# Kernel optimization log

Measured on AMD Instinct MI355X. Metric: run time of the kernel, lower is better.

Reference implementation:

```python
import jax, jax.numpy as jnp
import numpy as np

B, NPROP, NCLS, NPTS, NBQ, NCK = 32, 256, 19, 4096, 64, 64
C, QH, VQ = 256, 768, 8


def setup_inputs() -> dict:
    key = jax.random.key(0)
    ks = jax.random.split(key, 12)
    s = 0.02
    return dict(
        sem_cls_logits=jax.random.normal(ks[0], (B, NPROP, NCLS), jnp.float32),
        prop_features=jax.random.normal(ks[1], (B, NPROP, C), jnp.float32),
        box_corners=jax.random.normal(ks[2], (B, NPROP, 8, 3), jnp.float32),
        enc_xyz=jax.random.uniform(ks[3], (B, NPTS, 3), jnp.float32),
        enc_features=jax.random.normal(ks[4], (B, NPTS, C), jnp.float32),
        pc_min=jnp.zeros((B, 3), jnp.float32),
        pc_max=jnp.ones((B, 3), jnp.float32),
        box_query=jax.random.normal(ks[5], (B, NBQ, 8, 3), jnp.float32),
        box_qmask=jnp.ones((B, NBQ), jnp.float32),
        click_query=jax.random.uniform(ks[6], (B, NCK, 3), jnp.float32),
        click_qmask=jnp.ones((B, NCK), jnp.float32),
        gauss_B=jax.random.normal(ks[7], (3, C // 2), jnp.float32),
        box_w1=jax.random.normal(ks[8], (C, QH), jnp.float32) * s,
        box_b1=jnp.zeros((QH,), jnp.float32),
        box_w2=jax.random.normal(ks[9], (QH, VQ * QH), jnp.float32) * s,
        box_b2=jnp.zeros((VQ * QH,), jnp.float32),
        click_w1=jax.random.normal(ks[10], (2 * C, QH), jnp.float32) * s,
        click_b1=jnp.zeros((QH,), jnp.float32),
        click_w2=jax.random.normal(ks[11], (QH, VQ * QH), jnp.float32) * s,
        click_b2=jnp.zeros((VQ * QH,), jnp.float32),
    )


def _mlp(x, w1, b1, w2, b2):
    h = jax.nn.relu(jnp.einsum('bqc,ch->bqh', x, w1) + b1)
    return jnp.einsum('bqh,ho->bqo', h, w2) + b2


def _forward(sem_cls_logits, prop_features, box_corners, enc_xyz, enc_features,
             pc_min, pc_max, box_query, box_qmask, click_query, click_qmask,
             gauss_B, box_w1, box_b1, box_w2, box_b2,
             click_w1, click_b1, click_w2, click_b2):
    bsz = sem_cls_logits.shape[0]
    # proposal semantic mask: 0 for background (last class)
    prop_sem_mask = (jnp.argmax(sem_cls_logits, -1) != sem_cls_logits.shape[-1] - 1)
    prop_sem_mask = prop_sem_mask.astype(prop_features.dtype)  # [B, nprop]

    # ---- box branch: axis-aligned 3D IoU from box corners, argmax match, gather ----
    mn_p = box_corners.min(-2)  # [B, nprop, 3]
    mx_p = box_corners.max(-2)
    vol_p = jnp.prod(mx_p - mn_p, -1)  # [B, nprop]
    mn_q = box_query.min(-2)   # [B, nq, 3]
    mx_q = box_query.max(-2)
    vol_q = jnp.prod(mx_q - mn_q, -1)  # [B, nq]
    inter = jnp.prod(
        jnp.clip(jnp.minimum(mx_q[:, :, None], mx_p[:, None]) -
                 jnp.maximum(mn_q[:, :, None], mn_p[:, None]), 0.0, None), -1)  # [B,nq,nprop]
    iou = inter / (vol_q[:, :, None] + vol_p[:, None] - inter + 1e-8)
    iou = iou * prop_sem_mask[:, None, :]
    match_idx = jnp.argmax(iou, -1)  # [B, nq]
    box_feat = jnp.take_along_axis(prop_features, match_idx[..., None], axis=1)  # [B,nq,C]
    box_prompt = _mlp(box_feat, box_w1, box_b1, box_w2, box_b2).reshape(bsz, -1, QH)
    box_mask = jnp.repeat(box_qmask[:, :, None], VQ, axis=2).reshape(bsz, -1)

    # ---- click branch: fourier pos emb + nearest-neighbor gather + MLP ----
    xyz01 = (click_query - pc_min[:, None]) / (pc_max - pc_min)[:, None]
    proj = (xyz01 * (2.0 * jnp.pi)) @ gauss_B  # [B, nclick, C//2]
    pos = jnp.concatenate([jnp.sin(proj), jnp.cos(proj)], -1)  # [B, nclick, C]
    # squared distances (argmin equivalent to cdist argmin)
    d2 = jnp.sum((click_query[:, :, None, :] - enc_xyz[:, None, :, :]) ** 2, -1)  # [B,nclick,npts]
    nn_ids = jnp.argmin(d2, -1)  # [B, nclick]
    k_fea = jnp.take_along_axis(enc_features, nn_ids[..., None], axis=1)  # [B,nclick,C]
    click_in = jnp.concatenate([k_fea, pos], -1)  # [B, nclick, 2C]
    click_prompt = _mlp(click_in, click_w1, click_b1, click_w2, click_b2).reshape(bsz, -1, QH)
    click_mask = jnp.repeat(click_qmask[:, :, None], VQ, axis=2).reshape(bsz, -1)

    prompt_feature = jnp.concatenate([box_prompt, click_prompt], axis=1)  # [B,(nq+nclick)*VQ,QH]
    prompt_mask = jnp.concatenate([box_mask, click_mask], axis=1)
    return prompt_feature, prompt_mask


def reference(sem_cls_logits, prop_features, box_corners, enc_xyz, enc_features,
              pc_min, pc_max, box_query, box_qmask, click_query, click_qmask,
              gauss_B, box_w1, box_b1, box_w2, box_b2,
              click_w1, click_b1, click_w2, click_b2):
    return _forward(sem_cls_logits, prop_features, box_corners, enc_xyz, enc_features,
                    pc_min, pc_max, box_query, box_qmask, click_query, click_qmask,
                    gauss_B, box_w1, box_b1, box_w2, box_b2,
                    click_w1, click_b1, click_w2, click_b2)
```

## Files before the change

### kernel.cpp

```cpp
#include <hip/hip_runtime.h>

#define TWO_PI 6.283185307179586f

typedef _Float16 half8 __attribute__((ext_vector_type(8)));
typedef _Float16 half4 __attribute__((ext_vector_type(4)));
typedef float floatx4 __attribute__((ext_vector_type(4)));

__device__ __forceinline__ void async16(const _Float16* g, _Float16* l) {
    __builtin_amdgcn_global_load_lds(
        (const __attribute__((address_space(1))) void*)g,
        (__attribute__((address_space(3))) void*)l, 16, 0, 0);
}

__device__ __forceinline__ void transpose_core(
    const float* __restrict__ src, _Float16* __restrict__ dst,
    int K, int N, _Float16* t, int bx, int by)
{
    int n0 = bx * 64, k0 = by * 64;
    int tid = threadIdx.x;
    int r = tid >> 4;
    int c4 = (tid & 15) * 4;
#pragma unroll
    for (int p = 0; p < 4; p++) {
        int k = r + p*16;
        float4 v = *(const float4*)(src + (size_t)(k0+k)*N + n0 + c4);
        t[(c4+0)*68 + k] = (_Float16)v.x;
        t[(c4+1)*68 + k] = (_Float16)v.y;
        t[(c4+2)*68 + k] = (_Float16)v.z;
        t[(c4+3)*68 + k] = (_Float16)v.w;
    }
    __syncthreads();
    int ck = (tid & 15) * 4;
#pragma unroll
    for (int p = 0; p < 4; p++) {
        int n = r + p*16;
        half4 v = *(const half4*)(t + n*68 + ck);
        *(half4*)(dst + (size_t)(n0+n)*K + k0 + ck) = v;
    }
}

__global__ void mega_prep(
    const float* __restrict__ logits, const float* __restrict__ corners,
    const float* __restrict__ box_query,
    const float* __restrict__ bw1, const float* __restrict__ cw1,
    _Float16* __restrict__ w1t_box, _Float16* __restrict__ w1t_clk,
    const float* __restrict__ bw2, const float* __restrict__ cw2,
    _Float16* __restrict__ w2t_box, _Float16* __restrict__ w2t_clk,
    const float* __restrict__ prop_features,
    const float* __restrict__ enc_features,
    const float* __restrict__ enc_xyz,
    const float* __restrict__ cq,
    const float* __restrict__ pc_min,
    const float* __restrict__ pc_max,
    const float* __restrict__ gB,
    const float* __restrict__ box_qmask,
    const float* __restrict__ click_qmask,
    _Float16* __restrict__ box_in,
    _Float16* __restrict__ click_in,
    float* __restrict__ out)
{
    __shared__ float smem[2176];
    __shared__ float nnd[4]; __shared__ int nni[4];
    __shared__ float bxd[4]; __shared__ int bxi[4];
    __shared__ int s_nn, s_match;
    int bid = blockIdx.x;
    if (bid < 2304) {
        _Float16* tb = (_Float16*)smem;
        int x = bid % 96, y = (bid / 96) % 12, z = bid / 1152;
        if (z == 0) transpose_core(bw2, w2t_box, 768, 6144, tb, x, y);
        else        transpose_core(cw2, w2t_clk, 768, 6144, tb, x, y);
        return;
    }
    if (bid < 2496) {
        _Float16* tb = (_Float16*)smem;
        int r = bid - 2304;
        int x = r % 12, y = (r / 12) % 8, z = r / 96;
        if (z == 0) {
            if (y < 4) transpose_core(bw1, w1t_box, 256, 768, tb, x, y);
        } else {
            transpose_core(cw1, w1t_clk, 512, 768, tb, x, y);
        }
        return;
    }

    int row = bid - 2496;
    int t = threadIdx.x;
    int b = row >> 6;
    int lane = t & 63, wave = t >> 6;

    float cx = cq[row*3+0];
    float cy = cq[row*3+1];
    float cz = cq[row*3+2];
    const float* ex = enc_xyz + (size_t)b * 4096 * 3;
    float nbest = 3.4e38f; int nbidx = 0;
#pragma unroll
    for (int i = 0; i < 16; i++) {
        int p = t + i*256;
        float dx = cx - ex[p*3+0];
        float dy = cy - ex[p*3+1];
        float dz = cz - ex[p*3+2];
        float d = dx*dx + dy*dy;
        d = d + dz*dz;
        if (d < nbest) { nbest = d; nbidx = p; }
    }
#pragma unroll
    for (int off = 32; off; off >>= 1) {
        float ov = __shfl_down(nbest, off);
        int   oi = __shfl_down(nbidx, off);
        if (ov < nbest || (ov == nbest && oi < nbidx)) { nbest = ov; nbidx = oi; }
    }
    if (lane == 0) { nnd[wave] = nbest; nni[wave] = nbidx; }

    float iou; int pidx = t;
    {
        const float* c = corners + ((size_t)b*256 + t) * 24;
        float mn0 = c[0], mn1 = c[1], mn2 = c[2];
        float mx0 = mn0, mx1 = mn1, mx2 = mn2;
#pragma unroll
        for (int k = 1; k < 8; k++) {
            float v0 = c[k*3+0], v1 = c[k*3+1], v2 = c[k*3+2];
            mn0 = fminf(mn0, v0); mx0 = fmaxf(mx0, v0);
            mn1 = fminf(mn1, v1); mx1 = fmaxf(mx1, v1);
            mn2 = fminf(mn2, v2); mx2 = fmaxf(mx2, v2);
        }
        float pvol = (mx0-mn0)*(mx1-mn1)*(mx2-mn2);
        const float* lg = logits + ((size_t)b*256 + t) * 19;
        float bv = lg[0]; int bi = 0;
#pragma unroll
        for (int k = 1; k < 19; k++) { float v = lg[k]; if (v > bv) { bv = v; bi = k; } }
        float pmsk = (bi != 18) ? 1.0f : 0.0f;

        const float* qc = box_query + (size_t)row * 24;
        float qn0 = qc[0], qn1 = qc[1], qn2 = qc[2];
        float qx0 = qn0, qx1 = qn1, qx2 = qn2;
#pragma unroll
        for (int k = 1; k < 8; k++) {
            float v0 = qc[k*3+0], v1 = qc[k*3+1], v2 = qc[k*3+2];
            qn0 = fminf(qn0, v0); qx0 = fmaxf(qx0, v0);
            qn1 = fminf(qn1, v1); qx1 = fmaxf(qx1, v1);
            qn2 = fminf(qn2, v2); qx2 = fmaxf(qx2, v2);
        }
        float qvol = (qx0-qn0)*(qx1-qn1)*(qx2-qn2);
        float e0 = fminf(qx0, mx0) - fmaxf(qn0, mn0); e0 = fmaxf(e0, 0.0f);
        float e1 = fminf(qx1, mx1) - fmaxf(qn1, mn1); e1 = fmaxf(e1, 0.0f);
        float e2 = fminf(qx2, mx2) - fmaxf(qn2, mn2); e2 = fmaxf(e2, 0.0f);
        float inter = (e0*e1)*e2;
        iou = inter / (qvol + pvol - inter + 1e-8f) * pmsk;
    }
#pragma unroll
    for (int off = 32; off; off >>= 1) {
        float ov = __shfl_down(iou, off);
        int   oi = __shfl_down(pidx, off);
        if (ov > iou || (ov == iou && oi < pidx)) { iou = ov; pidx = oi; }
    }
    if (lane == 0) { bxd[wave] = iou; bxi[wave] = pidx; }
    __syncthreads();
    if (t == 0) {
        float nv = nnd[0]; int ni = nni[0];
        float bv = bxd[0]; int bi = bxi[0];
#pragma unroll
        for (int w = 1; w < 4; w++) {
            if (nnd[w] < nv || (nnd[w] == nv && nni[w] < ni)) { nv = nnd[w]; ni = nni[w]; }
            if (bxd[w] > bv || (bxd[w] == bv && bxi[w] < bi)) { bv = bxd[w]; bi = bxi[w]; }
        }
        s_nn = ni; s_match = bi;
    }
    __syncthreads();
    int nnid = s_nn, match = s_match;

    box_in[(size_t)row*256 + t] =
        (_Float16)prop_features[((size_t)b*256 + match)*256 + t];
    click_in[(size_t)row*512 + t] =
        (_Float16)enc_features[((size_t)b*4096 + nnid)*256 + t];
    int j = t & 127;
    float m0 = pc_min[b*3+0], m1 = pc_min[b*3+1], m2 = pc_min[b*3+2];
    float tx = (cx - m0) / (pc_max[b*3+0] - m0) * TWO_PI;
    float ty = (cy - m1) / (pc_max[b*3+1] - m1) * TWO_PI;
    float tz = (cz - m2) / (pc_max[b*3+2] - m2) * TWO_PI;
    float p = tx * gB[j] + ty * gB[128+j] + tz * gB[256+j];
    float v = (t < 128) ? sinf(p) : cosf(p);
    click_in[(size_t)row*512 + 256 + t] = (_Float16)v;
    if (t < 16) {
        int idx = row*16 + t;
        int mb = idx >> 10, i = idx & 1023;
        float mv = (i < 512) ? box_qmask[mb*64 + (i >> 3)]
                             : click_qmask[mb*64 + ((i - 512) >> 3)];
        out[25165824 + idx] = mv;
    }
}

template<int MODE>
__device__ __forceinline__ void gemm_core(
    const _Float16* __restrict__ A, const _Float16* __restrict__ Bt,
    const float* __restrict__ bias, int N, int K,
    _Float16* __restrict__ Hout, float* __restrict__ Fout, long brOff,
    int bm, int bn, _Float16* As, _Float16* Bs)
{
    const int tid = threadIdx.x;
    const int wave = tid >> 6, lane = tid & 63;
    const int waveM = (wave & 1) * 64, waveN = (wave >> 1) * 64;
    const int nrow = lane & 15;
    const int kq   = lane >> 4;

    const int srow = tid >> 3;
    const int jdat = ((tid & 7) ^ (srow & 7)) * 8;

    floatx4 acc[4][4];
#pragma unroll
    for (int i = 0; i < 4; i++)
#pragma unroll
        for (int j = 0; j < 4; j++) { floatx4 z = {0.f,0.f,0.f,0.f}; acc[i][j] = z; }

    const _Float16* Ab[4]; const _Float16* Bb[4];
    _Float16 *lA[4], *lB[4];
#pragma unroll
    for (int q = 0; q < 4; q++) {
        Ab[q] = A  + (size_t)(bm*128 + q*32 + srow) * K + jdat;
        Bb[q] = Bt + (size_t)(bn*128 + q*32 + srow) * K + jdat;
        lA[q] = As + q*2048 + wave*512;
        lB[q] = Bs + q*2048 + wave*512;
    }

    for (int kk = 0; kk < K; kk += 64) {
        __syncthreads();
#pragma unroll
        for (int q = 0; q < 4; q++) async16(Ab[q] + kk, lA[q]);
#pragma unroll
        for (int q = 0; q < 4; q++) async16(Bb[q] + kk, lB[q]);
        __syncthreads();
#pragma unroll
        for (int h = 0; h < 2; h++) {
            const int sw = (((kq + h*4) ^ (nrow & 7)) * 8);
            half8 af[4], bf[4];
#pragma unroll
            for (int i = 0; i < 4; i++)
                af[i] = *(const half8*)(As + (waveM + i*16 + nrow)*64 + sw);
#pragma unroll
            for (int j = 0; j < 4; j++)
                bf[j] = *(const half8*)(Bs + (waveN + j*16 + nrow)*64 + sw);
#pragma unroll
            for (int i = 0; i < 4; i++)
#pragma unroll
                for (int j = 0; j < 4; j++)
                    acc[i][j] = __builtin_amdgcn_mfma_f32_16x16x32_f16(af[i], bf[j], acc[i][j], 0, 0, 0);
        }
    }

#pragma unroll
    for (int i = 0; i < 4; i++) {
#pragma unroll
        for (int j = 0; j < 4; j++) {
            int col = bn*128 + waveN + j*16 + nrow;
            float bv = bias[col];
#pragma unroll
            for (int r = 0; r < 4; r++) {
                int row = bm*128 + waveM + i*16 + kq*4 + r;
                float v = acc[i][j][r] + bv;
                if (MODE == 0) {
                    v = v > 0.f ? v : 0.f;
                    Hout[(size_t)row * N + col] = (_Float16)v;
                } else {
                    size_t off = (size_t)(row >> 6) * 786432 + (size_t)brOff
                               + (size_t)(row & 63) * 6144 + col;
                    Fout[off] = v;
                }
            }
        }
    }
}

__global__ __launch_bounds__(256) void gemm_l1(
    const _Float16* __restrict__ A0, const _Float16* __restrict__ A1,
    const _Float16* __restrict__ B0, const _Float16* __restrict__ B1,
    const float* __restrict__ b0, const float* __restrict__ b1,
    _Float16* __restrict__ H0, _Float16* __restrict__ H1)
{
    __shared__ _Float16 As[8192];
    __shared__ _Float16 Bs[8192];
    if (blockIdx.z == 0)
        gemm_core<0>(A0, B0, b0, 768, 256, H0, nullptr, 0,
                     blockIdx.x, blockIdx.y, As, Bs);
    else
        gemm_core<0>(A1, B1, b1, 768, 512, H1, nullptr, 0,
                     blockIdx.x, blockIdx.y, As, Bs);
}

__global__ __launch_bounds__(256) void gemm_l2(
    const _Float16* __restrict__ A0, const _Float16* __restrict__ A1,
    const _Float16* __restrict__ B0, const _Float16* __restrict__ B1,
    const float* __restrict__ b0, const float* __restrict__ b1,
    float* __restrict__ out)
{
    __shared__ _Float16 As[8192];
    __shared__ _Float16 Bs[8192];
    int lin = blockIdx.x + 16 * blockIdx.y;
    int xcd = lin & 7;
    int per = lin >> 3;
    int bm  = per & 15;
    int bn  = xcd * 6 + (per >> 4);
    if (blockIdx.z == 0)
        gemm_core<1>(A0, B0, b0, 6144, 768, nullptr, out, 0,      bm, bn, As, Bs);
    else
        gemm_core<1>(A1, B1, b1, 6144, 768, nullptr, out, 393216, bm, bn, As, Bs);
}

extern "C" void kernel_launch(void* const* d_in, const int* in_sizes, int n_in,
                              void* d_out, int out_size, void* d_ws, size_t ws_size,
                              hipStream_t stream)
{
    const float* sem   = (const float*)d_in[0];
    const float* propf = (const float*)d_in[1];
    const float* boxc  = (const float*)d_in[2];
    const float* encx  = (const float*)d_in[3];
    const float* encf  = (const float*)d_in[4];
    const float* pcmin = (const float*)d_in[5];
    const float* pcmax = (const float*)d_in[6];
    const float* boxq  = (const float*)d_in[7];
    const float* boxm  = (const float*)d_in[8];
    const float* clkq  = (const float*)d_in[9];
    const float* clkm  = (const float*)d_in[10];
    const float* gB    = (const float*)d_in[11];
    const float* bw1   = (const float*)d_in[12];
    const float* bb1   = (const float*)d_in[13];
    const float* bw2   = (const float*)d_in[14];
    const float* bb2   = (const float*)d_in[15];
    const float* cw1   = (const float*)d_in[16];
    const float* cb1   = (const float*)d_in[17];
    const float* cw2   = (const float*)d_in[18];
    const float* cb2   = (const float*)d_in[19];
    float* out = (float*)d_out;
    char* ws = (char*)d_ws;

    _Float16* box_in   = (_Float16*)(ws + 278528);
    _Float16* click_in = (_Float16*)(ws + 1327104);
    _Float16* h_box    = (_Float16*)(ws + 3424256);
    _Float16* h_click  = (_Float16*)(ws + 6569984);
    _Float16* w1t_box  = (_Float16*)(ws + 9715712);
    _Float16* w2t_box  = (_Float16*)(ws + 10108928);
    _Float16* w1t_clk  = (_Float16*)(ws + 19546112);
    _Float16* w2t_clk  = (_Float16*)(ws + 20332544);

    mega_prep<<<4544, 256, 0, stream>>>(sem, boxc, boxq,
                                        bw1, cw1, w1t_box, w1t_clk,
                                        bw2, cw2, w2t_box, w2t_clk,
                                        propf, encf, encx, clkq,
                                        pcmin, pcmax, gB, boxm, clkm,
                                        box_in, click_in, out);
    gemm_l1<<<dim3(16, 6, 2),  256, 0, stream>>>(box_in, click_in, w1t_box, w1t_clk,
                                                 bb1, cb1, h_box, h_click);
    gemm_l2<<<dim3(16, 48, 2), 256, 0, stream>>>(h_box, h_click, w2t_box, w2t_clk,
                                                 bb2, cb2, out);
}
```

Measured before the change: 322.5 us.

## Use 256x256 double-buffered layer-2 GEMM and move W2 transpose into layer-1 launch

Layer 2 becomes a new 512-thread GEMM kernel with 256x256 output tiles, double-buffered LDS stages loaded asynchronously, and XCD-aware block remapping. The goal is more operand reuse and overlap of global loads with MFMA work. The W2 fp32-to-fp16 transpose moves out of the prep kernel and is co-scheduled with the small layer-1 GEMM, so prep gets shorter and the transpose can overlap with layer-1 compute. Costs are larger LDS use (128KB per block), more register pressure from 32 accumulators per thread, and fewer blocks for load balancing.

```diff
diff --git a/kernel.cpp b/kernel.cpp
--- a/kernel.cpp
+++ b/kernel.cpp
@@ -44,8 +44,6 @@
     const float* __restrict__ box_query,
     const float* __restrict__ bw1, const float* __restrict__ cw1,
     _Float16* __restrict__ w1t_box, _Float16* __restrict__ w1t_clk,
-    const float* __restrict__ bw2, const float* __restrict__ cw2,
-    _Float16* __restrict__ w2t_box, _Float16* __restrict__ w2t_clk,
     const float* __restrict__ prop_features,
     const float* __restrict__ enc_features,
     const float* __restrict__ enc_xyz,
@@ -64,17 +62,9 @@
     __shared__ float bxd[4]; __shared__ int bxi[4];
     __shared__ int s_nn, s_match;
     int bid = blockIdx.x;
-    if (bid < 2304) {
+    if (bid < 192) {
         _Float16* tb = (_Float16*)smem;
-        int x = bid % 96, y = (bid / 96) % 12, z = bid / 1152;
-        if (z == 0) transpose_core(bw2, w2t_box, 768, 6144, tb, x, y);
-        else        transpose_core(cw2, w2t_clk, 768, 6144, tb, x, y);
-        return;
-    }
-    if (bid < 2496) {
-        _Float16* tb = (_Float16*)smem;
-        int r = bid - 2304;
-        int x = r % 12, y = (r / 12) % 8, z = r / 96;
+        int x = bid % 12, y = (bid / 12) % 8, z = bid / 96;
         if (z == 0) {
             if (y < 4) transpose_core(bw1, w1t_box, 256, 768, tb, x, y);
         } else {
@@ -83,7 +73,7 @@
         return;
     }
 
-    int row = bid - 2496;
+    int row = bid - 192;
     int t = threadIdx.x;
     int b = row >> 6;
     int lane = t & 63, wave = t >> 6;
@@ -269,39 +259,153 @@
     }
 }
 
-__global__ __launch_bounds__(256) void gemm_l1(
+__global__ __launch_bounds__(256) void gemm_l1_t2(
     const _Float16* __restrict__ A0, const _Float16* __restrict__ A1,
     const _Float16* __restrict__ B0, const _Float16* __restrict__ B1,
     const float* __restrict__ b0, const float* __restrict__ b1,
-    _Float16* __restrict__ H0, _Float16* __restrict__ H1)
+    _Float16* __restrict__ H0, _Float16* __restrict__ H1,
+    const float* __restrict__ bw2, const float* __restrict__ cw2,
+    _Float16* __restrict__ w2t_box, _Float16* __restrict__ w2t_clk)
 {
     __shared__ _Float16 As[8192];
     __shared__ _Float16 Bs[8192];
-    if (blockIdx.z == 0)
-        gemm_core<0>(A0, B0, b0, 768, 256, H0, nullptr, 0,
-                     blockIdx.x, blockIdx.y, As, Bs);
-    else
-        gemm_core<0>(A1, B1, b1, 768, 512, H1, nullptr, 0,
-                     blockIdx.x, blockIdx.y, As, Bs);
-}
-
-__global__ __launch_bounds__(256) void gemm_l2(
+    int bid = blockIdx.x;
+    if (bid < 192) {
+        int z = bid / 96, r = bid % 96;
+        int bm = r % 16, bn = r / 16;
+        if (z == 0)
+            gemm_core<0>(A0, B0, b0, 768, 256, H0, nullptr, 0, bm, bn, As, Bs);
+        else
+            gemm_core<0>(A1, B1, b1, 768, 512, H1, nullptr, 0, bm, bn, As, Bs);
+    } else {
+        int r = bid - 192;
+        int x = r % 96, y = (r / 96) % 12, z = r / 1152;
+        if (z == 0) transpose_core(bw2, w2t_box, 768, 6144, As, x, y);
+        else        transpose_core(cw2, w2t_clk, 768, 6144, As, x, y);
+    }
+}
+
+__global__ __launch_bounds__(512, 2) void gemm_l2_8p(
     const _Float16* __restrict__ A0, const _Float16* __restrict__ A1,
     const _Float16* __restrict__ B0, const _Float16* __restrict__ B1,
     const float* __restrict__ b0, const float* __restrict__ b1,
     float* __restrict__ out)
 {
-    __shared__ _Float16 As[8192];
-    __shared__ _Float16 Bs[8192];
-    int lin = blockIdx.x + 16 * blockIdx.y;
-    int xcd = lin & 7;
-    int per = lin >> 3;
-    int bm  = per & 15;
-    int bn  = xcd * 6 + (per >> 4);
-    if (blockIdx.z == 0)
-        gemm_core<1>(A0, B0, b0, 6144, 768, nullptr, out, 0,      bm, bn, As, Bs);
-    else
-        gemm_core<1>(A1, B1, b1, 6144, 768, nullptr, out, 393216, bm, bn, As, Bs);
+    __shared__ _Float16 As[2][16384];
+    __shared__ _Float16 Bs[2][16384];
+
+    int lin = blockIdx.x;
+    int wg  = (lin & 7) * 48 + (lin >> 3);
+    int br  = wg / 192;
+    int r   = wg % 192;
+    int bn  = r >> 3;
+    int bm  = r & 7;
+    const _Float16* A  = br ? A1 : A0;
+    const _Float16* Bt = br ? B1 : B0;
+    const float* bias  = br ? b1 : b0;
+    long brOff = br ? 393216 : 0;
+
+    const int tid  = threadIdx.x;
+    const int wave = tid >> 6, lane = tid & 63;
+    const int waveM = (wave & 1) * 128;
+    const int waveN = (wave >> 1) * 64;
+    const int nrow = lane & 15;
+    const int kq   = lane >> 4;
+
+    const int srow = tid >> 3;
+    const int jdat = ((tid & 7) ^ (srow & 7)) * 8;
+    const int ldst = wave * 512;
+
+    const _Float16* Ag[4]; const _Float16* Bg[4];
+#pragma unroll
+    for (int q = 0; q < 4; q++) {
+        Ag[q] = A  + (size_t)(bm*256 + q*64 + srow) * 768 + jdat;
+        Bg[q] = Bt + (size_t)(bn*256 + q*64 + srow) * 768 + jdat;
+    }
+
+    floatx4 acc[8][4];
+#pragma unroll
+    for (int i = 0; i < 8; i++)
+#pragma unroll
+        for (int j = 0; j < 4; j++) { floatx4 z = {0.f,0.f,0.f,0.f}; acc[i][j] = z; }
+
+    const int sw0 = ((kq    ) ^ (nrow & 7)) * 8;
+    const int sw1 = ((kq + 4) ^ (nrow & 7)) * 8;
+    int aoff[8], boff[4];
+#pragma unroll
+    for (int i = 0; i < 8; i++) aoff[i] = (waveM + i*16 + nrow) * 64;
+#pragma unroll
+    for (int j = 0; j < 4; j++) boff[j] = (waveN + j*16 + nrow) * 64;
+
+#define STAGE_TILE(kk, c) do {                                        \
+    _Float16* asd = &As[c][0]; _Float16* bsd = &Bs[c][0];             \
+    _Pragma("unroll")                                                 \
+    for (int q = 0; q < 4; q++) async16(Ag[q] + (kk), asd + q*4096 + ldst); \
+    _Pragma("unroll")                                                 \
+    for (int q = 0; q < 4; q++) async16(Bg[q] + (kk), bsd + q*4096 + ldst); \
+} while (0)
+
+    STAGE_TILE(0, 0);
+    STAGE_TILE(64, 1);
+    asm volatile("s_waitcnt vmcnt(8)" ::: "memory");
+    __builtin_amdgcn_s_barrier();
+
+    for (int t = 0; t < 12; ++t) {
+        const int cur = t & 1;
+        const _Float16* as = &As[cur][0];
+        const _Float16* bs = &Bs[cur][0];
+        half8 bf[4][2];
+#pragma unroll
+        for (int j = 0; j < 4; j++) {
+            bf[j][0] = *(const half8*)(bs + boff[j] + sw0);
+            bf[j][1] = *(const half8*)(bs + boff[j] + sw1);
+        }
+#pragma unroll
+        for (int c = 0; c < 4; c++) {
+            half8 af[2][2];
+#pragma unroll
+            for (int m = 0; m < 2; m++) {
+                af[m][0] = *(const half8*)(as + aoff[2*c+m] + sw0);
+                af[m][1] = *(const half8*)(as + aoff[2*c+m] + sw1);
+            }
+            if (c == 3) {
+                asm volatile("s_waitcnt lgkmcnt(0)" ::: "memory");
+                __builtin_amdgcn_s_barrier();
+                if (t < 10) STAGE_TILE((t + 2) * 64, cur);
+            }
+            __builtin_amdgcn_s_setprio(1);
+#pragma unroll
+            for (int m = 0; m < 2; m++)
+#pragma unroll
+                for (int j = 0; j < 4; j++) {
+                    acc[2*c+m][j] = __builtin_amdgcn_mfma_f32_16x16x32_f16(
+                        af[m][0], bf[j][0], acc[2*c+m][j], 0, 0, 0);
+                    acc[2*c+m][j] = __builtin_amdgcn_mfma_f32_16x16x32_f16(
+                        af[m][1], bf[j][1], acc[2*c+m][j], 0, 0, 0);
+                }
+            __builtin_amdgcn_s_setprio(0);
+        }
+        if (t < 10) { asm volatile("s_waitcnt vmcnt(8)" ::: "memory"); }
+        else        { asm volatile("s_waitcnt vmcnt(0)" ::: "memory"); }
+        __builtin_amdgcn_s_barrier();
+    }
+#undef STAGE_TILE
+
+#pragma unroll
+    for (int i = 0; i < 8; i++) {
+#pragma unroll
+        for (int j = 0; j < 4; j++) {
+            int col = bn*256 + waveN + j*16 + nrow;
+            float bv = bias[col];
+#pragma unroll
+            for (int rr = 0; rr < 4; rr++) {
+                int row = bm*256 + waveM + i*16 + kq*4 + rr;
+                size_t off = (size_t)(row >> 6) * 786432 + (size_t)brOff
+                           + (size_t)(row & 63) * 6144 + col;
+                out[off] = acc[i][j][rr] + bv;
+            }
+        }
+    }
 }
 
 extern "C" void kernel_launch(void* const* d_in, const int* in_sizes, int n_in,
@@ -340,14 +444,14 @@
     _Float16* w1t_clk  = (_Float16*)(ws + 19546112);
     _Float16* w2t_clk  = (_Float16*)(ws + 20332544);
 
-    mega_prep<<<4544, 256, 0, stream>>>(sem, boxc, boxq,
+    mega_prep<<<2240, 256, 0, stream>>>(sem, boxc, boxq,
                                         bw1, cw1, w1t_box, w1t_clk,
-                                        bw2, cw2, w2t_box, w2t_clk,
                                         propf, encf, encx, clkq,
                                         pcmin, pcmax, gB, boxm, clkm,
                                         box_in, click_in, out);
-    gemm_l1<<<dim3(16, 6, 2),  256, 0, stream>>>(box_in, click_in, w1t_box, w1t_clk,
-                                                 bb1, cb1, h_box, h_click);
-    gemm_l2<<<dim3(16, 48, 2), 256, 0, stream>>>(h_box, h_click, w2t_box, w2t_clk,
-                                                 bb2, cb2, out);
-}
+    gemm_l1_t2<<<2496, 256, 0, stream>>>(box_in, click_in, w1t_box, w1t_clk,
+                                         bb1, cb1, h_box, h_click,
+                                         bw2, cw2, w2t_box, w2t_clk);
+    gemm_l2_8p<<<384, 512, 0, stream>>>(h_box, h_click, w2t_box, w2t_clk,
+                                        bb2, cb2, out);
+}
```

Result: no change. 323.3 us (+0.3%).

## Move W2 transpose from prep kernel into layer-1 GEMM launch

Applied to the files above, without the earlier changes.

The fp32-to-fp16 transpose of the large second-layer weights moves out of the prep kernel and into the layer-1 GEMM launch as extra blocks. The 192 GEMM blocks come first and the transpose blocks fill the GPU alongside them, so the small, under-occupied layer-1 GEMM overlaps with bandwidth-bound transpose work instead of running alone. The prep kernel shrinks to the W1 transpose and per-row work. The transpose now uses the GEMM's As shared buffer, which is sized to fit it.

```diff
diff --git a/kernel.cpp b/kernel.cpp
--- a/kernel.cpp
+++ b/kernel.cpp
@@ -44,8 +44,6 @@
     const float* __restrict__ box_query,
     const float* __restrict__ bw1, const float* __restrict__ cw1,
     _Float16* __restrict__ w1t_box, _Float16* __restrict__ w1t_clk,
-    const float* __restrict__ bw2, const float* __restrict__ cw2,
-    _Float16* __restrict__ w2t_box, _Float16* __restrict__ w2t_clk,
     const float* __restrict__ prop_features,
     const float* __restrict__ enc_features,
     const float* __restrict__ enc_xyz,
@@ -64,17 +62,9 @@
     __shared__ float bxd[4]; __shared__ int bxi[4];
     __shared__ int s_nn, s_match;
     int bid = blockIdx.x;
-    if (bid < 2304) {
+    if (bid < 192) {
         _Float16* tb = (_Float16*)smem;
-        int x = bid % 96, y = (bid / 96) % 12, z = bid / 1152;
-        if (z == 0) transpose_core(bw2, w2t_box, 768, 6144, tb, x, y);
-        else        transpose_core(cw2, w2t_clk, 768, 6144, tb, x, y);
-        return;
-    }
-    if (bid < 2496) {
-        _Float16* tb = (_Float16*)smem;
-        int r = bid - 2304;
-        int x = r % 12, y = (r / 12) % 8, z = r / 96;
+        int x = bid % 12, y = (bid / 12) % 8, z = bid / 96;
         if (z == 0) {
             if (y < 4) transpose_core(bw1, w1t_box, 256, 768, tb, x, y);
         } else {
@@ -83,7 +73,7 @@
         return;
     }
 
-    int row = bid - 2496;
+    int row = bid - 192;
     int t = threadIdx.x;
     int b = row >> 6;
     int lane = t & 63, wave = t >> 6;
@@ -269,20 +259,30 @@
     }
 }
 
-__global__ __launch_bounds__(256) void gemm_l1(
+__global__ __launch_bounds__(256) void gemm_l1_t2(
     const _Float16* __restrict__ A0, const _Float16* __restrict__ A1,
     const _Float16* __restrict__ B0, const _Float16* __restrict__ B1,
     const float* __restrict__ b0, const float* __restrict__ b1,
-    _Float16* __restrict__ H0, _Float16* __restrict__ H1)
+    _Float16* __restrict__ H0, _Float16* __restrict__ H1,
+    const float* __restrict__ bw2, const float* __restrict__ cw2,
+    _Float16* __restrict__ w2t_box, _Float16* __restrict__ w2t_clk)
 {
     __shared__ _Float16 As[8192];
     __shared__ _Float16 Bs[8192];
-    if (blockIdx.z == 0)
-        gemm_core<0>(A0, B0, b0, 768, 256, H0, nullptr, 0,
-                     blockIdx.x, blockIdx.y, As, Bs);
-    else
-        gemm_core<0>(A1, B1, b1, 768, 512, H1, nullptr, 0,
-                     blockIdx.x, blockIdx.y, As, Bs);
+    int bid = blockIdx.x;
+    if (bid < 192) {
+        int z = bid / 96, r = bid % 96;
+        int bm = r % 16, bn = r / 16;
+        if (z == 0)
+            gemm_core<0>(A0, B0, b0, 768, 256, H0, nullptr, 0, bm, bn, As, Bs);
+        else
+            gemm_core<0>(A1, B1, b1, 768, 512, H1, nullptr, 0, bm, bn, As, Bs);
+    } else {
+        int r = bid - 192;
+        int x = r % 96, y = (r / 96) % 12, z = r / 1152;
+        if (z == 0) transpose_core(bw2, w2t_box, 768, 6144, As, x, y);
+        else        transpose_core(cw2, w2t_clk, 768, 6144, As, x, y);
+    }
 }
 
 __global__ __launch_bounds__(256) void gemm_l2(
@@ -340,14 +340,14 @@
     _Float16* w1t_clk  = (_Float16*)(ws + 19546112);
     _Float16* w2t_clk  = (_Float16*)(ws + 20332544);
 
-    mega_prep<<<4544, 256, 0, stream>>>(sem, boxc, boxq,
+    mega_prep<<<2240, 256, 0, stream>>>(sem, boxc, boxq,
                                         bw1, cw1, w1t_box, w1t_clk,
-                                        bw2, cw2, w2t_box, w2t_clk,
                                         propf, encf, encx, clkq,
                                         pcmin, pcmax, gB, boxm, clkm,
                                         box_in, click_in, out);
-    gemm_l1<<<dim3(16, 6, 2),  256, 0, stream>>>(box_in, click_in, w1t_box, w1t_clk,
-                                                 bb1, cb1, h_box, h_click);
+    gemm_l1_t2<<<2496, 256, 0, stream>>>(box_in, click_in, w1t_box, w1t_clk,
+                                         bb1, cb1, h_box, h_click,
+                                         bw2, cw2, w2t_box, w2t_clk);
     gemm_l2<<<dim3(16, 48, 2), 256, 0, stream>>>(h_box, h_click, w2t_box, w2t_clk,
                                                  bb2, cb2, out);
 }
```

After: 316.8 us. No clear change (-1.7%).
